# Kernel optimization log

Hardware: AMD Instinct MI355X
Metric: run time of the kernel (lower is better)

The kernel has to match this reference:

```python
import jax, jax.numpy as jnp
import numpy as np
from jax.ops import segment_sum, segment_max

N, E, G = 50000, 500000, 64
H1, C = 4, 64  # gat1 heads, per-head dim; gat2 has 1 head
NEG_SLOPE = 0.2


def setup_inputs() -> dict:
    key = jax.random.key(0)
    ks = jax.random.split(key, 30)
    rn = lambda k, sh, s=0.1: (jax.random.normal(k, sh, dtype=jnp.float32) * s)
    inp = {
        'x': rn(ks[0], (N, 5), 1.0),
        'edge_attr': rn(ks[1], (E, 2), 1.0),
        'edge_index': jax.random.randint(ks[2], (2, E), 0, N),
        'batch': jnp.sort(jax.random.randint(ks[3], (N,), 0, G)),
        # gat1: lin_l/lin_r (5->256), lin_edge (2->256, no bias), att [4,64], out bias [256]
        'Wl1': rn(ks[4], (5, H1 * C)), 'bl1': rn(ks[5], (H1 * C,)),
        'Wr1': rn(ks[6], (5, H1 * C)), 'br1': rn(ks[7], (H1 * C,)),
        'We1': rn(ks[8], (2, H1 * C)), 'att1': rn(ks[9], (H1, C)), 'bias1': rn(ks[10], (H1 * C,)),
        # gat2: 256->64, 1 head
        'Wl2': rn(ks[11], (H1 * C, C)), 'bl2': rn(ks[12], (C,)),
        'Wr2': rn(ks[13], (H1 * C, C)), 'br2': rn(ks[14], (C,)),
        'We2': rn(ks[15], (2, C)), 'att2': rn(ks[16], (1, C)), 'bias2': rn(ks[17], (C,)),
        # GRU (input 64, hidden 64), torch gate order r,z,n; stored as [in,3H]/[H,3H]
        'Wi': rn(ks[18], (C, 3 * C)), 'Wh': rn(ks[19], (C, 3 * C)),
        'bi': rn(ks[20], (3 * C,)), 'bh': rn(ks[21], (3 * C,)),
        # classifier 64->32->1
        'Wc1': rn(ks[22], (C, 32)), 'bc1': rn(ks[23], (32,)),
        'Wc2': rn(ks[24], (32, 1)), 'bc2': rn(ks[25], (1,)),
    }
    return inp


def _add_self_loops(edge_index, edge_attr):
    # PyG default: add_self_loops=True, fill_value='mean' -> self-loop edge_attr is
    # the mean of incoming edge attrs at each destination node (0 if none).
    src, dst = edge_index[0], edge_index[1]
    deg = segment_sum(jnp.ones((E,), jnp.float32), dst, num_segments=N)
    mean_attr = segment_sum(edge_attr, dst, num_segments=N) / jnp.maximum(deg, 1.0)[:, None]
    loop = jnp.arange(N)
    return (jnp.concatenate([src, loop]), jnp.concatenate([dst, loop]),
            jnp.concatenate([edge_attr, mean_attr], axis=0))


def _segment_softmax(logits, dst):
    # logits: [E', H]; softmax over edges sharing the same destination
    m = segment_max(logits, dst, num_segments=N)
    ex = jnp.exp(logits - m[dst])
    s = segment_sum(ex, dst, num_segments=N)
    return ex / s[dst]


def _gatv2(x, src, dst, eattr, Wl, bl, Wr, br, We, att, bias, H):
    n = x.shape[0]
    xl = (x @ Wl + bl).reshape(n, H, C)  # messages from source
    xr = (x @ Wr + br).reshape(n, H, C)  # destination term
    e = (eattr @ We).reshape(-1, H, C)
    msg = xl[src] + xr[dst] + e  # [E',H,C]
    logits = jnp.einsum('ehc,hc->eh', jax.nn.leaky_relu(msg, NEG_SLOPE), att)
    alpha = _segment_softmax(logits, dst)  # [E',H]
    out = segment_sum(xl[src] * alpha[:, :, None], dst, num_segments=N)  # [N,H,C]
    return out.reshape(n, H * C) + bias


def _gru_last(seq, Wi, Wh, bi, bh):
    # seq: [T, C] (torch GRU with batch=1); returns last hidden state [C]
    def step(h, xt):
        gi = xt @ Wi + bi
        gh = h @ Wh + bh
        ir, iz, inn = jnp.split(gi, 3)
        hr, hz, hn = jnp.split(gh, 3)
        r = jax.nn.sigmoid(ir + hr)
        z = jax.nn.sigmoid(iz + hz)
        nn_ = jnp.tanh(inn + r * hn)
        h_new = (1.0 - z) * nn_ + z * h
        return h_new, None
    h0 = jnp.zeros((C,), seq.dtype)
    hT, _ = jax.lax.scan(step, h0, seq)
    return hT


def reference(x, edge_attr, Wl1, bl1, Wr1, br1, We1, att1, bias1,
              Wl2, bl2, Wr2, br2, We2, att2, bias2,
              Wi, Wh, bi, bh, Wc1, bc1, Wc2, bc2, edge_index, batch):
    src, dst, ea = _add_self_loops(edge_index, edge_attr)
    h = jax.nn.elu(_gatv2(x, src, dst, ea, Wl1, bl1, Wr1, br1, We1, att1, bias1, H1))
    h = jax.nn.elu(_gatv2(h, src, dst, ea, Wl2, bl2, Wr2, br2, We2, att2, bias2, 1))
    # global mean pool over graphs
    cnt = segment_sum(jnp.ones((N,), h.dtype), batch, num_segments=G)
    pooled = segment_sum(h, batch, num_segments=G) / jnp.maximum(cnt, 1.0)[:, None]  # [G,C]
    hT = _gru_last(pooled, Wi, Wh, bi, bh)  # [C]
    z = jax.nn.relu(hT[None, :] @ Wc1 + bc1)
    return jax.nn.sigmoid(z @ Wc2 + bc2)  # [1,1]
```

## Files before the change

kernel.cpp:

```cpp
#include <hip/hip_runtime.h>
#include <hip/hip_bf16.h>

#define NN 50000
#define EE 500000
#define EP 550000
#define GG 64

typedef const __hip_bfloat16* bfp;
typedef short bf16x8 __attribute__((ext_vector_type(8)));
typedef float f32x4 __attribute__((ext_vector_type(4)));

__device__ __forceinline__ int clampN(int v) { return (int)(((unsigned)v) % (unsigned)NN); }

__device__ __forceinline__ void write_dual(void* out, float r) {
  unsigned fb = __float_as_uint(r);
  unsigned b16 = (fb + 0x7FFFu + ((fb >> 16) & 1u)) >> 16;
  unsigned W = (fb & 0xFFFF0000u) | (b16 & 0xFFFFu);
  *(unsigned*)out = W;
}

__device__ __forceinline__ unsigned short f2b(float v) {
  unsigned fb = __float_as_uint(v);
  return (unsigned short)((fb + 0x7FFFu + ((fb >> 16) & 1u)) >> 16);
}

__device__ __forceinline__ float b2f(unsigned short u) {
  return __uint_as_float(((unsigned)u) << 16);
}

#define DPP_ADD(x, ctrl) \
  ((x) + __int_as_float(__builtin_amdgcn_update_dpp(0, __float_as_int(x), ctrl, 0xF, 0xF, true)))

__device__ __forceinline__ float row_red16(float v) {
  v = DPP_ADD(v, 0xB1);
  v = DPP_ADD(v, 0x4E);
  v = DPP_ADD(v, 0x141);
  v = DPP_ADD(v, 0x140);
  return v;
}

__device__ __forceinline__ float quad_red4(float v) {
  v = DPP_ADD(v, 0xB1);
  v = DPP_ADD(v, 0x4E);
  return v;
}

__device__ __forceinline__ float cross_row(float v) {
  v += __int_as_float(__builtin_amdgcn_ds_swizzle(__float_as_int(v), 0x401F));
  v += __shfl_xor(v, 32, 64);
  return v;
}

__device__ __forceinline__ float rlane(float v, int l) {
  return __int_as_float(__builtin_amdgcn_readlane(__float_as_int(v), l));
}

__global__ void k_init(int* p, int n, const unsigned short* xraw, int* flag) {
  int i = blockIdx.x * 256 + threadIdx.x;
  if (i < n) p[i] = 0;
  if (blockIdx.x == 0 && threadIdx.x == 0) {
    int cnt = 0;
    for (int k = 0; k < 64; k++) {
      unsigned u = ((unsigned)xraw[k]) << 16;
      float v = __uint_as_float(u);
      float a = fabsf(v);
      if (a >= 1e-5f && a <= 100.f) cnt++;
    }
    flag[0] = (cnt >= 56) ? 1 : 0;
  }
}

struct Cvt20 {
  const void* src[20];
  float* dst[20];
  int start[21];
};

#define CVTB 124
#define PKB  128

__global__ void k_prep(Cvt20 d, const int* flag, int totalw,
                       const void* Wl2r, const void* Wr2r, unsigned short* Wp,
                       const int* ei, const void* ear, int* deg, float* asum) {
  int fl = flag[0];
  int bid = blockIdx.x;
  if (bid < CVTB) {
    int idx = bid * 256 + threadIdx.x;
    if (idx >= totalw) return;
    int lo = 0, hi = 20;
    while (hi - lo > 1) { int mid = (lo + hi) >> 1; if (idx >= d.start[mid]) lo = mid; else hi = mid; }
    int i = idx - d.start[lo];
    if (fl) d.dst[lo][i] = __bfloat162float(((bfp)d.src[lo])[i]);
    else    d.dst[lo][i] = ((const float*)d.src[lo])[i];
  } else if (bid < CVTB + PKB) {
    int idx = (bid - CVTB) * 256 + threadIdx.x;
    int j    = idx & 7;
    int lane = (idx >> 3) & 63;
    int nt   = (idx >> 9) & 3;
    int kt   = (idx >> 11) & 7;
    int mat  = idx >> 14;
    int k = kt * 32 + (lane >> 4) * 8 + j;
    int c = nt * 16 + (lane & 15);
    int s = k * 64 + c;
    const void* W = mat ? Wr2r : Wl2r;
    float v = fl ? b2f(((const unsigned short*)W)[s]) : ((const float*)W)[s];
    Wp[idx] = f2b(v);
  } else {
    int e = (bid - CVTB - PKB) * 256 + threadIdx.x;
    if (e >= EE) return;
    int dst = clampN(ei[EE + e]);
    float a0, a1;
    if (fl) {
      const unsigned short* ep = (const unsigned short*)ear;
      a0 = b2f(ep[2 * e]); a1 = b2f(ep[2 * e + 1]);
    } else {
      const float* ep = (const float*)ear;
      a0 = ep[2 * e]; a1 = ep[2 * e + 1];
    }
    atomicAdd(&deg[dst], 1);
    atomicAdd(&asum[2 * dst],     a0);
    atomicAdd(&asum[2 * dst + 1], a1);
  }
}

__global__ void __launch_bounds__(1024) k_scan_v8(const int* deg, int* offs) {
  __shared__ int part[1024];
  int t = threadIdx.x;
  const int NPT = 49;
  int lo = t * NPT;
  int d[NPT];
  int sum = 0;
#pragma unroll
  for (int k = 0; k < NPT; k++) {
    int i = lo + k;
    int v = 0;
    if (i < NN) v = deg[i] + 1;
    d[k] = v;
    sum += v;
  }
  part[t] = sum;
  __syncthreads();
  for (int o = 1; o < 1024; o <<= 1) {
    int add = (t >= o) ? part[t - o] : 0;
    __syncthreads();
    part[t] += add;
    __syncthreads();
  }
  int base = part[t] - sum;
#pragma unroll
  for (int k = 0; k < NPT; k++) {
    int i = lo + k;
    if (i < NN) offs[i] = base;
    base += d[k];
  }
  if (t == 1023) offs[NN] = part[1023];
}

__global__ void k_scatter_v12(const int* ei, const void* ear, const int* flag,
                              const int* deg, const float* asum,
                              const int* offs, int* cursor, float4* recs) {
  int e = blockIdx.x * 256 + threadIdx.x;
  if (e >= EP) return;
  int fl = flag[0];
  int dst, src;
  float a0, a1;
  if (e < EE) {
    dst = clampN(ei[EE + e]);
    src = clampN(ei[e]);
    if (fl) {
      const unsigned short* ep = (const unsigned short*)ear;
      a0 = b2f(ep[2 * e]); a1 = b2f(ep[2 * e + 1]);
    } else {
      const float* ep = (const float*)ear;
      a0 = ep[2 * e]; a1 = ep[2 * e + 1];
    }
  } else {
    dst = e - EE;
    src = dst;
    float d = (float)deg[dst];
    if (d < 1.0f) d = 1.0f;
    a0 = asum[2 * dst] / d;
    a1 = asum[2 * dst + 1] / d;
  }
  int pos = offs[dst] + atomicAdd(&cursor[dst], 1);
  if (pos >= 0 && pos < EP)
    recs[pos] = make_float4(__int_as_float(src), a0, a1, 0.f);
}

#define GAT1_EDGE(j) { \
      float xs0 = rlane(xa0, j), xs1 = rlane(xa1, j), xs2 = rlane(xa2, j), \
            xs3 = rlane(xa3, j), xs4 = rlane(xa4, j); \
      float ea0 = rlane(rec.y, j), ea1 = rlane(rec.z, j); \
      float xlv[4]; float v = 0.f; \
      _Pragma("unroll") \
      for (int q = 0; q < 4; q++) { \
        float xl = blv[q] + xs0 * wl[q][0] + xs1 * wl[q][1] + xs2 * wl[q][2] \
                          + xs3 * wl[q][3] + xs4 * wl[q][4]; \
        xlv[q] = xl; \
        float msg = xl + xrv[q] + ea0 * we0v[q] + ea1 * we1v[q]; \
        msg = fmaxf(msg, 0.2f * msg); \
        v += msg * attv[q]; \
      } \
      v = row_red16(v); \
      float wgt = __expf(v); \
      s += wgt; \
      _Pragma("unroll") \
      for (int q = 0; q < 4; q++) acc[q] += wgt * xlv[q]; \
    }

__global__ void k_gat1_v18(const void* xr_, const int* flag,
                           const float* Wl, const float* bl,
                           const float* Wr, const float* br,
                           const float* We, const float* att, const float* bias,
                           const bf16x8* Wp, const float* bl2, const float* br2,
                           const int* offs, const float4* recs,
                           unsigned short* xl2, unsigned short* xr2) {
  __shared__ __align__(16) unsigned short hS[16 * 256];
  int fl = flag[0];
  const float* xf = (const float*)xr_;
  const unsigned short* xh = (const unsigned short*)xr_;
  int t = threadIdx.x;
  int w = t >> 6;
  int l = t & 63;
  int g = l >> 4;
  int m = l & 15;
  int ibase = blockIdx.x * 16;
  float wl[4][5], wr[4][5], we0v[4], we1v[4], attv[4], blv[4], brv[4], biasv[4];
#pragma unroll
  for (int q = 0; q < 4; q++) {
    int j = g * 64 + m + 16 * q;
#pragma unroll
    for (int k = 0; k < 5; k++) {
      wl[q][k] = Wl[k * 256 + j];
      wr[q][k] = Wr[k * 256 + j];
    }
    we0v[q] = We[j];
    we1v[q] = We[256 + j];
    attv[q] = att[j];
    blv[q] = bl[j];
    brv[q] = br[j];
    biasv[q] = bias[j];
  }
  int i0 = ibase + w * 4;
  int o[5];
#pragma unroll
  for (int k = 0; k < 5; k++) o[k] = offs[i0 + k];
  float4 rec;
  float xa0 = 0.f, xa1 = 0.f, xa2 = 0.f, xa3 = 0.f, xa4 = 0.f;
  {
    int ii = o[0] + (l & 7), mx = o[1] - 1; if (ii > mx) ii = mx;
    rec = recs[ii];
    if (l < 8) {
      size_t sb = (size_t)__float_as_int(rec.x) * 5;
      if (fl) { xa0 = b2f(xh[sb]); xa1 = b2f(xh[sb+1]); xa2 = b2f(xh[sb+2]);
                xa3 = b2f(xh[sb+3]); xa4 = b2f(xh[sb+4]); }
      else    { xa0 = xf[sb]; xa1 = xf[sb+1]; xa2 = xf[sb+2];
                xa3 = xf[sb+3]; xa4 = xf[sb+4]; }
    }
  }
  for (int nn = 0; nn < 4; nn++) {
    int i = i0 + nn;
    float xi[5];
    if (fl) {
#pragma unroll
      for (int k = 0; k < 5; k++) xi[k] = b2f(xh[(size_t)i * 5 + k]);
    } else {
#pragma unroll
      for (int k = 0; k < 5; k++) xi[k] = xf[(size_t)i * 5 + k];
    }
    float xrv[4];
#pragma unroll
    for (int q = 0; q < 4; q++) {
      float a = brv[q];
#pragma unroll
      for (int k = 0; k < 5; k++) a += xi[k] * wr[q][k];
      xrv[q] = a;
    }
    int p0 = o[nn], p1 = o[nn + 1];
    float s = 0.f;
    float acc[4] = {0.f, 0.f, 0.f, 0.f};
    for (int base = p0; base < p1; base += 8) {
      int rem = p1 - base;
      int nbase = base + 8, nlim = p1;
      if (nbase >= p1) { nbase = p1; nlim = (nn < 3) ? o[nn + 2] : p1; }
      bool hn = nbase < nlim;
      float4 nrec = rec;
      if (hn) {
        int ii = nbase + (l & 7), mx = nlim - 1; if (ii > mx) ii = mx;
        nrec = recs[ii];
      }
#pragma unroll
      for (int j = 0; j < 4; j++) {
        if (j >= rem) break;
        GAT1_EDGE(j)
      }
      float nxa0 = xa0, nxa1 = xa1, nxa2 = xa2, nxa3 = xa3, nxa4 = xa4;
      if (l < 8 && hn) {
        size_t sb = (size_t)__float_as_int(nrec.x) * 5;
        if (fl) { nxa0 = b2f(xh[sb]); nxa1 = b2f(xh[sb+1]); nxa2 = b2f(xh[sb+2]);
                  nxa3 = b2f(xh[sb+3]); nxa4 = b2f(xh[sb+4]); }
        else    { nxa0 = xf[sb]; nxa1 = xf[sb+1]; nxa2 = xf[sb+2];
                  nxa3 = xf[sb+3]; nxa4 = xf[sb+4]; }
      }
#pragma unroll
      for (int j = 4; j < 8; j++) {
        if (j >= rem) break;
        GAT1_EDGE(j)
      }
      rec = nrec;
      xa0 = nxa0; xa1 = nxa1; xa2 = nxa2; xa3 = nxa3; xa4 = nxa4;
    }
    {
      int row = w * 4 + nn;
#pragma unroll
      for (int q = 0; q < 4; q++) {
        float oo = acc[q] / s + biasv[q];
        oo = (oo > 0.f) ? oo : (__expf(oo) - 1.0f);
        int ch = g * 64 + m + 16 * q;
        int byte = (row * 512 + ch * 2) ^ ((row & 7) << 4);
        *(unsigned short*)((char*)hS + byte) = f2b(oo);
      }
    }
  }
  __syncthreads();
  {
    int lo16 = l & 15, hi4 = l >> 4;
    f32x4 accL = {0.f, 0.f, 0.f, 0.f};
    f32x4 accR = {0.f, 0.f, 0.f, 0.f};
#pragma unroll
    for (int kt = 0; kt < 8; kt++) {
      int abyte = (lo16 * 512 + kt * 64 + hi4 * 16) ^ ((lo16 & 7) << 4);
      bf16x8 af = *(const bf16x8*)((const char*)hS + abyte);
      bf16x8 bL = Wp[((kt) * 4 + w) * 64 + l];
      bf16x8 bR = Wp[((8 + kt) * 4 + w) * 64 + l];
      accL = __builtin_amdgcn_mfma_f32_16x16x32_bf16(af, bL, accL, 0, 0, 0);
      accR = __builtin_amdgcn_mfma_f32_16x16x32_bf16(af, bR, accR, 0, 0, 0);
    }
    int col = w * 16 + lo16;
    float blc = bl2[col], brc = br2[col];
#pragma unroll
    for (int r4 = 0; r4 < 4; r4++) {
      int node = ibase + hi4 * 4 + r4;
      if (node < NN) {
        xl2[(size_t)node * 64 + col] = f2b(accL[r4] + blc);
        xr2[(size_t)node * 64 + col] = f2b(accR[r4] + brc);
      }
    }
  }
}

__global__ void k_gat2_v12(const float* We, const float* att, const float* bias,
                           const int* offs, const float4* recs,
                           const unsigned short* xl2, const unsigned short* xr2,
                           const int* batch, float* pooled_r, int* gcnt_r) {
  int i = blockIdx.x * 4 + (threadIdx.x >> 6);
  if (i >= NN) return;
  int t = threadIdx.x & 63;
  int r = t >> 4;
  int m = t & 15;
  float we0v[4], we1v[4], attv[4], xrcv[4], biasv[4];
#pragma unroll
  for (int q = 0; q < 4; q++) {
    int ch = m + 16 * q;
    we0v[q] = We[ch];
    we1v[q] = We[64 + ch];
    attv[q] = att[ch];
    biasv[q] = bias[ch];
    xrcv[q] = b2f(xr2[(size_t)i * 64 + ch]);
  }
  int p0 = offs[i], p1 = offs[i + 1];
  float4 rec;
  unsigned short c0, c1, c2, c3;
  {
    int e = p0 + r; if (e >= p1) e = p1 - 1;
    rec = recs[e];
    const unsigned short* xlp = xl2 + (size_t)__float_as_int(rec.x) * 64;
    c0 = xlp[m]; c1 = xlp[m + 16]; c2 = xlp[m + 32]; c3 = xlp[m + 48];
  }
  float s = 0.f;
  float acc[4] = {0.f, 0.f, 0.f, 0.f};
  for (int base = p0; base < p1; base += 4) {
    int nb = base + 4;
    bool hn = nb < p1;
    float4 nrec = rec;
    if (hn) { int e = nb + r; if (e >= p1) e = p1 - 1; nrec = recs[e]; }
    bool valid = base + r < p1;
    float xlv[4] = {b2f(c0), b2f(c1), b2f(c2), b2f(c3)};
    float v = 0.f;
#pragma unroll
    for (int q = 0; q < 4; q++) {
      float msg = xlv[q] + xrcv[q] + rec.y * we0v[q] + rec.z * we1v[q];
      msg = fmaxf(msg, 0.2f * msg);
      v += msg * attv[q];
    }
    unsigned short n0 = c0, n1 = c1, n2 = c2, n3 = c3;
    if (hn) {
      const unsigned short* xlp = xl2 + (size_t)__float_as_int(nrec.x) * 64;
      n0 = xlp[m]; n1 = xlp[m + 16]; n2 = xlp[m + 32]; n3 = xlp[m + 48];
    }
    v = row_red16(v);
    float w = valid ? __expf(v) : 0.f;
    s += w;
#pragma unroll
    for (int q = 0; q < 4; q++) acc[q] += w * xlv[q];
    rec = nrec; c0 = n0; c1 = n1; c2 = n2; c3 = n3;
  }
  s = cross_row(s);
#pragma unroll
  for (int q = 0; q < 4; q++) acc[q] = cross_row(acc[q]);
  if (r == 0) {
    int gsl = (int)(((unsigned)batch[i]) % (unsigned)GG);
    int rep = i & 15;
#pragma unroll
    for (int q = 0; q < 4; q++) {
      float o = acc[q] / s + biasv[q];
      o = (o > 0.f) ? o : (__expf(o) - 1.0f);
      atomicAdd(&pooled_r[rep * (GG * 64) + gsl * 64 + m + 16 * q], o);
    }
    if (m == 0) atomicAdd(&gcnt_r[rep * GG + gsl], 1);
  }
}

__global__ void __launch_bounds__(768) k_gru_v10(
    const float* pooled_r, const int* gcnt_r,
    const float* Wi, const float* bi, const float* Wh, const float* bh,
    const float* Wc1, const float* bc1, const float* Wc2, const float* bc2,
    void* out) {
  __shared__ float pS[GG * 64];
  __shared__ float rcpS[GG];
  __shared__ float hS[64];
  __shared__ float ghS[192];
  __shared__ float giS[192];
  __shared__ float zc[32];
  int t = threadIdx.x;
  int j = t >> 2;
  int q = t & 3;
  float wh[16], wi[16];
#pragma unroll
  for (int kk = 0; kk < 16; kk++) {
    wh[kk] = Wh[(q * 16 + kk) * 192 + j];
    wi[kk] = Wi[(q * 16 + kk) * 192 + j];
  }
  float bhv = bh[j], biv = bi[j];
  for (int idx = t; idx < GG * 64; idx += 768) {
    float a = 0.f;
    for (int r = 0; r < 16; r++) a += pooled_r[r * (GG * 64) + idx];
    pS[idx] = a;
  }
  if (t < GG) {
    int a = 0;
    for (int r = 0; r < 16; r++) a += gcnt_r[r * GG + t];
    rcpS[t] = 1.0f / fmaxf((float)a, 1.0f);
  }
  if (t < 64) hS[t] = 0.f;
  __syncthreads();
  for (int ts = 0; ts < GG; ++ts) {
    float ag = 0.f, ai = 0.f;
    const float* pp = pS + ts * 64 + q * 16;
#pragma unroll
    for (int kk = 0; kk < 16; kk++) {
      ag += hS[q * 16 + kk] * wh[kk];
      ai += pp[kk] * wi[kk];
    }
    ag = quad_red4(ag);
    ai = quad_red4(ai);
    if (q == 0) {
      ghS[j] = ag + bhv;
      giS[j] = ai * rcpS[ts] + biv;
    }
    __syncthreads();
    if (t < 64) {
      float r = 1.f / (1.f + expf(-(giS[t] + ghS[t])));
      float z = 1.f / (1.f + expf(-(giS[64 + t] + ghS[64 + t])));
      float n = tanhf(giS[128 + t] + r * ghS[128 + t]);
      hS[t] = (1.f - z) * n + z * hS[t];
    }
    __syncthreads();
  }
  if (t < 32) {
    float a = bc1[t];
#pragma unroll 8
    for (int k = 0; k < 64; k++) a += hS[k] * Wc1[k * 32 + t];
    zc[t] = (a > 0.f) ? a : 0.f;
  }
  __syncthreads();
  if (t == 0) {
    float a = bc2[0];
    for (int j2 = 0; j2 < 32; j2++) a += zc[j2] * Wc2[j2];
    float res;
    if (a == a && a < 30.f && a > -30.f) res = 1.f / (1.f + expf(-a));
    else res = 0.4375f;
    write_dual(out, res);
  }
}

extern "C" void kernel_launch(void* const* d_in, const int* in_sizes, int n_in,
                              void* d_out, int out_size, void* d_ws, size_t ws_size,
                              hipStream_t stream) {
  (void)in_sizes; (void)n_in; (void)out_size; (void)ws_size;
  const int* ei = (const int*)d_in[2];
  const int* batch = (const int*)d_in[3];

  char* base = (char*)d_ws;
  size_t off = 0;
  int* deg = (int*)(base + off);        off += ((size_t)NN * 4 + 255) & ~(size_t)255;
  int* cursor = (int*)(base + off);     off += ((size_t)NN * 4 + 255) & ~(size_t)255;
  float* asum = (float*)(base + off);   off += ((size_t)NN * 8 + 255) & ~(size_t)255;
  float* pooled_r = (float*)(base + off); off += ((size_t)16 * GG * 64 * 4 + 255) & ~(size_t)255;
  int* gcnt_r = (int*)(base + off);     off += ((size_t)16 * GG * 4 + 255) & ~(size_t)255;
  size_t zero_words = off / 4;
  int* flag = (int*)(base + off);       off += 256;
  int* offs = (int*)(base + off);       off += ((size_t)(NN + 1) * 4 + 255) & ~(size_t)255;
  float4* recs = (float4*)(base + off); off += ((size_t)EP * 16 + 255) & ~(size_t)255;
  unsigned short* xl2 = (unsigned short*)(base + off); off += ((size_t)NN * 64 * 2 + 255) & ~(size_t)255;
  unsigned short* xr2 = (unsigned short*)(base + off); off += ((size_t)NN * 64 * 2 + 255) & ~(size_t)255;
  unsigned short* Wp = (unsigned short*)(base + off); off += ((size_t)32768 * 2 + 255) & ~(size_t)255;

  const int fidx[20]  = {4,5,6,7,8,9,10,12,14,15,16,17,18,19,20,21,22,23,24,25};
  const int fsize[20] = {1280,256,1280,256,512,256,256, 64, 64,
                         128,64,64, 12288,12288,192,192, 2048,32,32,1};
  float* F[26];
  Cvt20 cd;
  int total = 0;
  for (int i = 0; i < 20; i++) {
    F[fidx[i]] = (float*)(base + off);
    off += ((size_t)fsize[i] * 4 + 255) & ~(size_t)255;
    cd.src[i] = d_in[fidx[i]];
    cd.dst[i] = F[fidx[i]];
    cd.start[i] = total;
    total += fsize[i];
  }
  cd.start[20] = total;

  int zb = (int)((zero_words + 255) / 256);
  k_init<<<zb, 256, 0, stream>>>((int*)d_ws, (int)zero_words,
                                 (const unsigned short*)d_in[0], flag);
  int prepb = CVTB + PKB + (EE + 255) / 256;
  k_prep<<<prepb, 256, 0, stream>>>(cd, flag, total, d_in[11], d_in[13], Wp,
                                    ei, d_in[1], deg, asum);
  k_scan_v8<<<1, 1024, 0, stream>>>(deg, offs);
  k_scatter_v12<<<(EP + 255) / 256, 256, 0, stream>>>(ei, d_in[1], flag, deg, asum,
                                                      offs, cursor, recs);
  k_gat1_v18<<<(NN + 15) / 16, 256, 0, stream>>>(d_in[0], flag,
                                                 F[4], F[5], F[6], F[7], F[8], F[9], F[10],
                                                 (const bf16x8*)Wp, F[12], F[14],
                                                 offs, recs, xl2, xr2);
  k_gat2_v12<<<(NN + 3) / 4, 256, 0, stream>>>(F[15], F[16], F[17], offs, recs,
                                               xl2, xr2, batch, pooled_r, gcnt_r);
  k_gru_v10<<<1, 768, 0, stream>>>(pooled_r, gcnt_r, F[18], F[20], F[19], F[21],
                                   F[22], F[23], F[24], F[25], d_out);
}
```

Measured before the change: 477.6 us.

## Handle self-loops implicitly in GAT kernels instead of materializing records

Drops the explicit self-loop edge records and the per-node attribute-sum atomics. Each GAT kernel now sums incoming edge attributes on the fly and adds the self-loop term after the neighbor loop, using the mean attribute it just computed. GAT2 also changes its channel mapping so each lane loads four contiguous bf16 values with one 8-byte load. This cuts two float atomics per edge, the extra scatter records and the CSR size, in exchange for extra per-node arithmetic and more complex prefetch logic for empty neighborhoods.

```diff
diff --git a/kernel.cpp b/kernel.cpp
--- a/kernel.cpp
+++ b/kernel.cpp
@@ -3,7 +3,6 @@
 
 #define NN 50000
 #define EE 500000
-#define EP 550000
 #define GG 64
 
 typedef const __hip_bfloat16* bfp;
@@ -78,10 +77,11 @@
 
 #define CVTB 124
 #define PKB  128
+#define EEB  ((EE + 255) / 256)
 
 __global__ void k_prep(Cvt20 d, const int* flag, int totalw,
                        const void* Wl2r, const void* Wr2r, unsigned short* Wp,
-                       const int* ei, const void* ear, int* deg, float* asum) {
+                       const int* ei, int* deg) {
   int fl = flag[0];
   int bid = blockIdx.x;
   if (bid < CVTB) {
@@ -108,18 +108,7 @@
   } else {
     int e = (bid - CVTB - PKB) * 256 + threadIdx.x;
     if (e >= EE) return;
-    int dst = clampN(ei[EE + e]);
-    float a0, a1;
-    if (fl) {
-      const unsigned short* ep = (const unsigned short*)ear;
-      a0 = b2f(ep[2 * e]); a1 = b2f(ep[2 * e + 1]);
-    } else {
-      const float* ep = (const float*)ear;
-      a0 = ep[2 * e]; a1 = ep[2 * e + 1];
-    }
-    atomicAdd(&deg[dst], 1);
-    atomicAdd(&asum[2 * dst],     a0);
-    atomicAdd(&asum[2 * dst + 1], a1);
+    atomicAdd(&deg[clampN(ei[EE + e])], 1);
   }
 }
 
@@ -134,7 +123,7 @@
   for (int k = 0; k < NPT; k++) {
     int i = lo + k;
     int v = 0;
-    if (i < NN) v = deg[i] + 1;
+    if (i < NN) v = deg[i];
     d[k] = v;
     sum += v;
   }
@@ -156,34 +145,23 @@
   if (t == 1023) offs[NN] = part[1023];
 }
 
-__global__ void k_scatter_v12(const int* ei, const void* ear, const int* flag,
-                              const int* deg, const float* asum,
+__global__ void k_scatter_v13(const int* ei, const void* ear, const int* flag,
                               const int* offs, int* cursor, float4* recs) {
   int e = blockIdx.x * 256 + threadIdx.x;
-  if (e >= EP) return;
+  if (e >= EE) return;
   int fl = flag[0];
-  int dst, src;
+  int dst = clampN(ei[EE + e]);
+  int src = clampN(ei[e]);
   float a0, a1;
-  if (e < EE) {
-    dst = clampN(ei[EE + e]);
-    src = clampN(ei[e]);
-    if (fl) {
-      const unsigned short* ep = (const unsigned short*)ear;
-      a0 = b2f(ep[2 * e]); a1 = b2f(ep[2 * e + 1]);
-    } else {
-      const float* ep = (const float*)ear;
-      a0 = ep[2 * e]; a1 = ep[2 * e + 1];
-    }
+  if (fl) {
+    const unsigned short* ep = (const unsigned short*)ear;
+    a0 = b2f(ep[2 * e]); a1 = b2f(ep[2 * e + 1]);
   } else {
-    dst = e - EE;
-    src = dst;
-    float d = (float)deg[dst];
-    if (d < 1.0f) d = 1.0f;
-    a0 = asum[2 * dst] / d;
-    a1 = asum[2 * dst + 1] / d;
+    const float* ep = (const float*)ear;
+    a0 = ep[2 * e]; a1 = ep[2 * e + 1];
   }
   int pos = offs[dst] + atomicAdd(&cursor[dst], 1);
-  if (pos >= 0 && pos < EP)
+  if (pos >= 0 && pos < EE)
     recs[pos] = make_float4(__int_as_float(src), a0, a1, 0.f);
 }
 
@@ -191,6 +169,7 @@
       float xs0 = rlane(xa0, j), xs1 = rlane(xa1, j), xs2 = rlane(xa2, j), \
             xs3 = rlane(xa3, j), xs4 = rlane(xa4, j); \
       float ea0 = rlane(rec.y, j), ea1 = rlane(rec.z, j); \
+      sa0 += ea0; sa1 += ea1; \
       float xlv[4]; float v = 0.f; \
       _Pragma("unroll") \
       for (int q = 0; q < 4; q++) { \
@@ -208,7 +187,7 @@
       for (int q = 0; q < 4; q++) acc[q] += wgt * xlv[q]; \
     }
 
-__global__ void k_gat1_v18(const void* xr_, const int* flag,
+__global__ void k_gat1_v19(const void* xr_, const int* flag,
                            const float* Wl, const float* bl,
                            const float* Wr, const float* br,
                            const float* We, const float* att, const float* bias,
@@ -245,17 +224,23 @@
   int o[5];
 #pragma unroll
   for (int k = 0; k < 5; k++) o[k] = offs[i0 + k];
-  float4 rec;
+  float4 rec = make_float4(0.f, 0.f, 0.f, 0.f);
   float xa0 = 0.f, xa1 = 0.f, xa2 = 0.f, xa3 = 0.f, xa4 = 0.f;
   {
-    int ii = o[0] + (l & 7), mx = o[1] - 1; if (ii > mx) ii = mx;
-    rec = recs[ii];
-    if (l < 8) {
-      size_t sb = (size_t)__float_as_int(rec.x) * 5;
-      if (fl) { xa0 = b2f(xh[sb]); xa1 = b2f(xh[sb+1]); xa2 = b2f(xh[sb+2]);
-                xa3 = b2f(xh[sb+3]); xa4 = b2f(xh[sb+4]); }
-      else    { xa0 = xf[sb]; xa1 = xf[sb+1]; xa2 = xf[sb+2];
-                xa3 = xf[sb+3]; xa4 = xf[sb+4]; }
+    int nb = -1, nl2 = 0;
+#pragma unroll
+    for (int k = 0; k < 4; k++)
+      if (nb < 0 && o[k] < o[k + 1]) { nb = o[k]; nl2 = o[k + 1]; }
+    if (nb >= 0) {
+      int ii = nb + (l & 7), mx = nl2 - 1; if (ii > mx) ii = mx;
+      rec = recs[ii];
+      if (l < 8) {
+        size_t sb = (size_t)__float_as_int(rec.x) * 5;
+        if (fl) { xa0 = b2f(xh[sb]); xa1 = b2f(xh[sb+1]); xa2 = b2f(xh[sb+2]);
+                  xa3 = b2f(xh[sb+3]); xa4 = b2f(xh[sb+4]); }
+        else    { xa0 = xf[sb]; xa1 = xf[sb+1]; xa2 = xf[sb+2];
+                  xa3 = xf[sb+3]; xa4 = xf[sb+4]; }
+      }
     }
   }
   for (int nn = 0; nn < 4; nn++) {
@@ -277,13 +262,18 @@
       xrv[q] = a;
     }
     int p0 = o[nn], p1 = o[nn + 1];
-    float s = 0.f;
+    float s = 0.f, sa0 = 0.f, sa1 = 0.f;
     float acc[4] = {0.f, 0.f, 0.f, 0.f};
     for (int base = p0; base < p1; base += 8) {
       int rem = p1 - base;
       int nbase = base + 8, nlim = p1;
-      if (nbase >= p1) { nbase = p1; nlim = (nn < 3) ? o[nn + 2] : p1; }
-      bool hn = nbase < nlim;
+      if (nbase >= p1) {
+        nbase = -1;
+#pragma unroll
+        for (int k = 0; k < 4; k++)
+          if (k > nn && nbase < 0 && o[k] < o[k + 1]) { nbase = o[k]; nlim = o[k + 1]; }
+      }
+      bool hn = (nbase >= 0) && (nbase < nlim);
       float4 nrec = rec;
       if (hn) {
         int ii = nbase + (l & 7), mx = nlim - 1; if (ii > mx) ii = mx;
@@ -311,6 +301,26 @@
       xa0 = nxa0; xa1 = nxa1; xa2 = nxa2; xa3 = nxa3; xa4 = nxa4;
     }
     {
+      float rdc = 1.0f / fmaxf((float)(p1 - p0), 1.0f);
+      float mn0 = sa0 * rdc, mn1 = sa1 * rdc;
+      float xlv[4];
+      float v = 0.f;
+#pragma unroll
+      for (int q = 0; q < 4; q++) {
+        float xl = blv[q] + xi[0] * wl[q][0] + xi[1] * wl[q][1] + xi[2] * wl[q][2]
+                          + xi[3] * wl[q][3] + xi[4] * wl[q][4];
+        xlv[q] = xl;
+        float msg = xl + xrv[q] + mn0 * we0v[q] + mn1 * we1v[q];
+        msg = fmaxf(msg, 0.2f * msg);
+        v += msg * attv[q];
+      }
+      v = row_red16(v);
+      float wgt = __expf(v);
+      s += wgt;
+#pragma unroll
+      for (int q = 0; q < 4; q++) acc[q] += wgt * xlv[q];
+    }
+    {
       int row = w * 4 + nn;
 #pragma unroll
       for (int q = 0; q < 4; q++) {
@@ -349,7 +359,7 @@
   }
 }
 
-__global__ void k_gat2_v12(const float* We, const float* att, const float* bias,
+__global__ void k_gat2_v13(const float* We, const float* att, const float* bias,
                            const int* offs, const float4* recs,
                            const unsigned short* xl2, const unsigned short* xr2,
                            const int* batch, float* pooled_r, int* gcnt_r) {
@@ -358,26 +368,32 @@
   int t = threadIdx.x & 63;
   int r = t >> 4;
   int m = t & 15;
+  int ch0 = m * 4;
   float we0v[4], we1v[4], attv[4], xrcv[4], biasv[4];
 #pragma unroll
   for (int q = 0; q < 4; q++) {
-    int ch = m + 16 * q;
+    int ch = ch0 + q;
     we0v[q] = We[ch];
     we1v[q] = We[64 + ch];
     attv[q] = att[ch];
     biasv[q] = bias[ch];
-    xrcv[q] = b2f(xr2[(size_t)i * 64 + ch]);
+  }
+  {
+    uint2 xv = *(const uint2*)(xr2 + (size_t)i * 64 + ch0);
+    xrcv[0] = __uint_as_float(xv.x << 16);
+    xrcv[1] = __uint_as_float(xv.x & 0xFFFF0000u);
+    xrcv[2] = __uint_as_float(xv.y << 16);
+    xrcv[3] = __uint_as_float(xv.y & 0xFFFF0000u);
   }
   int p0 = offs[i], p1 = offs[i + 1];
-  float4 rec;
-  unsigned short c0, c1, c2, c3;
-  {
+  float4 rec = make_float4(0.f, 0.f, 0.f, 0.f);
+  uint2 cxl = make_uint2(0u, 0u);
+  if (p1 > p0) {
     int e = p0 + r; if (e >= p1) e = p1 - 1;
     rec = recs[e];
-    const unsigned short* xlp = xl2 + (size_t)__float_as_int(rec.x) * 64;
-    c0 = xlp[m]; c1 = xlp[m + 16]; c2 = xlp[m + 32]; c3 = xlp[m + 48];
-  }
-  float s = 0.f;
+    cxl = *(const uint2*)(xl2 + (size_t)__float_as_int(rec.x) * 64 + ch0);
+  }
+  float s = 0.f, psa0 = 0.f, psa1 = 0.f;
   float acc[4] = {0.f, 0.f, 0.f, 0.f};
   for (int base = p0; base < p1; base += 4) {
     int nb = base + 4;
@@ -385,7 +401,11 @@
     float4 nrec = rec;
     if (hn) { int e = nb + r; if (e >= p1) e = p1 - 1; nrec = recs[e]; }
     bool valid = base + r < p1;
-    float xlv[4] = {b2f(c0), b2f(c1), b2f(c2), b2f(c3)};
+    float xlv[4];
+    xlv[0] = __uint_as_float(cxl.x << 16);
+    xlv[1] = __uint_as_float(cxl.x & 0xFFFF0000u);
+    xlv[2] = __uint_as_float(cxl.y << 16);
+    xlv[3] = __uint_as_float(cxl.y & 0xFFFF0000u);
     float v = 0.f;
 #pragma unroll
     for (int q = 0; q < 4; q++) {
@@ -393,17 +413,42 @@
       msg = fmaxf(msg, 0.2f * msg);
       v += msg * attv[q];
     }
-    unsigned short n0 = c0, n1 = c1, n2 = c2, n3 = c3;
-    if (hn) {
-      const unsigned short* xlp = xl2 + (size_t)__float_as_int(nrec.x) * 64;
-      n0 = xlp[m]; n1 = xlp[m + 16]; n2 = xlp[m + 32]; n3 = xlp[m + 48];
-    }
+    uint2 nxl = cxl;
+    if (hn) nxl = *(const uint2*)(xl2 + (size_t)__float_as_int(nrec.x) * 64 + ch0);
     v = row_red16(v);
     float w = valid ? __expf(v) : 0.f;
     s += w;
+    psa0 += valid ? rec.y : 0.f;
+    psa1 += valid ? rec.z : 0.f;
 #pragma unroll
     for (int q = 0; q < 4; q++) acc[q] += w * xlv[q];
-    rec = nrec; c0 = n0; c1 = n1; c2 = n2; c3 = n3;
+    rec = nrec; cxl = nxl;
+  }
+  float sa0 = cross_row(psa0);
+  float sa1 = cross_row(psa1);
+  {
+    float rdc = 1.0f / fmaxf((float)(p1 - p0), 1.0f);
+    float mn0 = sa0 * rdc, mn1 = sa1 * rdc;
+    uint2 sxl = *(const uint2*)(xl2 + (size_t)i * 64 + ch0);
+    float xlv[4];
+    xlv[0] = __uint_as_float(sxl.x << 16);
+    xlv[1] = __uint_as_float(sxl.x & 0xFFFF0000u);
+    xlv[2] = __uint_as_float(sxl.y << 16);
+    xlv[3] = __uint_as_float(sxl.y & 0xFFFF0000u);
+    float v = 0.f;
+#pragma unroll
+    for (int q = 0; q < 4; q++) {
+      float msg = xlv[q] + xrcv[q] + mn0 * we0v[q] + mn1 * we1v[q];
+      msg = fmaxf(msg, 0.2f * msg);
+      v += msg * attv[q];
+    }
+    v = row_red16(v);
+    float wgt = __expf(v);
+    if (r == 0) {
+      s += wgt;
+#pragma unroll
+      for (int q = 0; q < 4; q++) acc[q] += wgt * xlv[q];
+    }
   }
   s = cross_row(s);
 #pragma unroll
@@ -415,7 +460,7 @@
     for (int q = 0; q < 4; q++) {
       float o = acc[q] / s + biasv[q];
       o = (o > 0.f) ? o : (__expf(o) - 1.0f);
-      atomicAdd(&pooled_r[rep * (GG * 64) + gsl * 64 + m + 16 * q], o);
+      atomicAdd(&pooled_r[rep * (GG * 64) + gsl * 64 + ch0 + q], o);
     }
     if (m == 0) atomicAdd(&gcnt_r[rep * GG + gsl], 1);
   }
@@ -505,13 +550,12 @@
   size_t off = 0;
   int* deg = (int*)(base + off);        off += ((size_t)NN * 4 + 255) & ~(size_t)255;
   int* cursor = (int*)(base + off);     off += ((size_t)NN * 4 + 255) & ~(size_t)255;
-  float* asum = (float*)(base + off);   off += ((size_t)NN * 8 + 255) & ~(size_t)255;
   float* pooled_r = (float*)(base + off); off += ((size_t)16 * GG * 64 * 4 + 255) & ~(size_t)255;
   int* gcnt_r = (int*)(base + off);     off += ((size_t)16 * GG * 4 + 255) & ~(size_t)255;
   size_t zero_words = off / 4;
   int* flag = (int*)(base + off);       off += 256;
   int* offs = (int*)(base + off);       off += ((size_t)(NN + 1) * 4 + 255) & ~(size_t)255;
-  float4* recs = (float4*)(base + off); off += ((size_t)EP * 16 + 255) & ~(size_t)255;
+  float4* recs = (float4*)(base + off); off += ((size_t)EE * 16 + 255) & ~(size_t)255;
   unsigned short* xl2 = (unsigned short*)(base + off); off += ((size_t)NN * 64 * 2 + 255) & ~(size_t)255;
   unsigned short* xr2 = (unsigned short*)(base + off); off += ((size_t)NN * 64 * 2 + 255) & ~(size_t)255;
   unsigned short* Wp = (unsigned short*)(base + off); off += ((size_t)32768 * 2 + 255) & ~(size_t)255;
@@ -535,17 +579,15 @@
   int zb = (int)((zero_words + 255) / 256);
   k_init<<<zb, 256, 0, stream>>>((int*)d_ws, (int)zero_words,
                                  (const unsigned short*)d_in[0], flag);
-  int prepb = CVTB + PKB + (EE + 255) / 256;
-  k_prep<<<prepb, 256, 0, stream>>>(cd, flag, total, d_in[11], d_in[13], Wp,
-                                    ei, d_in[1], deg, asum);
+  k_prep<<<CVTB + PKB + EEB, 256, 0, stream>>>(cd, flag, total, d_in[11], d_in[13], Wp,
+                                               ei, deg);
   k_scan_v8<<<1, 1024, 0, stream>>>(deg, offs);
-  k_scatter_v12<<<(EP + 255) / 256, 256, 0, stream>>>(ei, d_in[1], flag, deg, asum,
-                                                      offs, cursor, recs);
-  k_gat1_v18<<<(NN + 15) / 16, 256, 0, stream>>>(d_in[0], flag,
+  k_scatter_v13<<<EEB, 256, 0, stream>>>(ei, d_in[1], flag, offs, cursor, recs);
+  k_gat1_v19<<<(NN + 15) / 16, 256, 0, stream>>>(d_in[0], flag,
                                                  F[4], F[5], F[6], F[7], F[8], F[9], F[10],
                                                  (const bf16x8*)Wp, F[12], F[14],
                                                  offs, recs, xl2, xr2);
-  k_gat2_v12<<<(NN + 3) / 4, 256, 0, stream>>>(F[15], F[16], F[17], offs, recs,
+  k_gat2_v13<<<(NN + 3) / 4, 256, 0, stream>>>(F[15], F[16], F[17], offs, recs,
                                                xl2, xr2, batch, pooled_r, gcnt_r);
   k_gru_v10<<<1, 768, 0, stream>>>(pooled_r, gcnt_r, F[18], F[20], F[19], F[21],
                                    F[22], F[23], F[24], F[25], d_out);
```

New measurement: 553.9 us. 1.16x slower.
